# Kernel tuning notes

Hardware: AMD Instinct MI355X
Metric: run time of the kernel (lower is better)

Reference implementation:

```python
import jax, jax.numpy as jnp
import numpy as np

LAMBDA_G, LAMBDA_F, TAU, MIU_NU_OTHER = 1.938, 1.912, 3.5, 0.19
EPS = 1e-8

B, N, C, D = 8, 1000, 4000, 128  # batch, n_points, n_customers, embed_dim


def setup_inputs() -> dict:
    key = jax.random.key(0)
    ks = jax.random.split(key, 12)
    return {
        "embeddings": jax.random.normal(ks[0], (B, N, D), dtype=jnp.float32),
        "chosen_count": jax.random.randint(ks[1], (B, N), 0, 3, dtype=jnp.int32),
        "u_lj_reg": jax.random.uniform(ks[2], (B, N, C), dtype=jnp.float32),
        "u_lj_food": jax.random.uniform(ks[3], (B, N, C), dtype=jnp.float32),
        "u0": jax.random.uniform(ks[4], (B, C), dtype=jnp.float32),
        "pop": jax.random.uniform(ks[5], (B, C, 1), dtype=jnp.float32),
        "delivery_distances_reg_set": jax.random.uniform(ks[6], (B, N, 1), dtype=jnp.float32),
        "delivery_distances_food_set": jax.random.uniform(ks[7], (B, N, 1), dtype=jnp.float32),
        "fixed_cost_point": jax.random.uniform(ks[8], (B, 1, N), dtype=jnp.float32),
        "W": jax.random.normal(ks[9], (D, D), dtype=jnp.float32) * (1.0 / np.sqrt(D)),
        "b": jax.random.normal(ks[10], (D,), dtype=jnp.float32) * 0.01,
    }


def reference(embeddings, chosen_count, u_lj_reg, u_lj_food, u0, pop,
              delivery_distances_reg_set, delivery_distances_food_set,
              fixed_cost_point, W, b):
    batch_size, n_points = chosen_count.shape
    regular = (chosen_count >= 1).astype(jnp.float32)            # [B,N]
    food = (chosen_count >= 2).astype(jnp.float32)
    reg_cand = 1.0 - regular
    food_cand = regular - food

    # bmm(u^T, diag(mask)) == column-scale: u_reg[b,c,j] = u[b,j,c] * mask[b,j]
    u_reg = jnp.swapaxes(u_lj_reg, 1, 2) * reg_cand[:, None, :]   # [B,C,N]
    P_reg = u0[..., None] + u_reg + EPS
    revenue_g = jnp.sum(pop * (u_reg / P_reg) * LAMBDA_G, axis=1)  # [B,N]

    u_food = jnp.swapaxes(u_lj_food, 1, 2) * food_cand[:, None, :]
    P_food = u0[..., None] + u_food + EPS
    revenue_f = jnp.sum(pop * (u_food / P_food) * LAMBDA_F, axis=1)

    fcp = fixed_cost_point.reshape(batch_size, n_points)
    del_reg = TAU * (reg_cand * delivery_distances_reg_set[..., 0]) / 1000.0
    fix_reg = reg_cand * fcp
    del_food = TAU * (food_cand * delivery_distances_food_set[..., 0]) / 1000.0
    fix_food = food_cand * fcp

    revenue = revenue_g + revenue_f
    delivery = del_reg + del_food
    fixed = fix_reg + fix_food
    labor = 0.075 * revenue
    land = 0.005 * revenue
    advantage = revenue * MIU_NU_OTHER - labor - land - delivery - fixed
    reward_improve = jnp.clip(advantage, 0.0) / 100.0

    loc_best_soft = jax.nn.softmax(reward_improve, axis=-1)       # [B,N]
    context = jnp.einsum('bnd,bn->bd', embeddings, loc_best_soft)  # [B,D]
    return context @ W.T + b
```

## Files before the change

kernel.cpp:

```cpp
#include <hip/hip_runtime.h>

#define LAMBDA_G 1.938f
#define LAMBDA_F 1.912f
#define TAU_C    3.5f
#define EPSV     1e-8f

constexpr int B = 8, N = 1000, C = 4000, D = 128;
constexpr int S = 25, RPB = 40, RPT = 5;

__device__ __forceinline__ float waveReduceSum(float v) {
#pragma unroll
    for (int off = 32; off > 0; off >>= 1)
        v += __shfl_down(v, off, 64);
    return v;
}

__device__ __forceinline__ float waveReduceMax(float v) {
#pragma unroll
    for (int off = 32; off > 0; off >>= 1)
        v = fmaxf(v, __shfl_down(v, off, 64));
    return v;
}

__global__ __launch_bounds__(256) void reward_kernel(
    const float* __restrict__ u_reg, const float* __restrict__ u_food,
    const float* __restrict__ u0,    const float* __restrict__ pop,
    const int*   __restrict__ chosen,
    const float* __restrict__ dd_reg, const float* __restrict__ dd_food,
    const float* __restrict__ fcp,   float* __restrict__ reward)
{
    const int bj = blockIdx.x;
    const int b  = bj / N;
    const int t  = threadIdx.x;
    const int cc = chosen[bj];

    if (cc >= 2) {
        if (t == 0) reward[bj] = 0.0f;
        return;
    }

    const float* __restrict__ u    = (cc == 0 ? u_reg : u_food) + (size_t)bj * C;
    const float* __restrict__ u0b  = u0  + (size_t)b * C;
    const float* __restrict__ popb = pop + (size_t)b * C;
    const float  lam = (cc == 0) ? LAMBDA_G : LAMBDA_F;
    const float  dd  = (cc == 0) ? dd_reg[bj] : dd_food[bj];

    float acc = 0.0f;
    const float4* u4  = (const float4*)u;
    const float4* u04 = (const float4*)u0b;
    const float4* p4  = (const float4*)popb;
    for (int c4 = t; c4 < C / 4; c4 += 256) {
        float4 uv = u4[c4];
        float4 ov = u04[c4];
        float4 pv = p4[c4];
        acc += pv.x * uv.x / (ov.x + uv.x + EPSV);
        acc += pv.y * uv.y / (ov.y + uv.y + EPSV);
        acc += pv.z * uv.z / (ov.z + uv.z + EPSV);
        acc += pv.w * uv.w / (ov.w + uv.w + EPSV);
    }

    __shared__ float red[4];
    float ws = waveReduceSum(acc);
    if ((t & 63) == 0) red[t >> 6] = ws;
    __syncthreads();
    if (t == 0) {
        float s       = red[0] + red[1] + red[2] + red[3];
        float revenue = lam * s;
        float delivery = TAU_C * dd * (1.0f / 1000.0f);
        float fixedc   = fcp[bj];
        float adv = revenue * 0.19f - 0.075f * revenue - 0.005f * revenue
                    - delivery - fixedc;
        reward[bj] = fmaxf(adv, 0.0f) * 0.01f;
    }
}

__global__ __launch_bounds__(256) void softmax_kernel(
    const float* __restrict__ reward, float* __restrict__ e_out)
{
    const int b = blockIdx.x;
    const int t = threadIdx.x;

    __shared__ float e[N];
    __shared__ float red[4];

    const float* __restrict__ r = reward + b * N;

    float m = -1e30f;
    for (int j = t; j < N; j += 256) m = fmaxf(m, r[j]);
    m = waveReduceMax(m);
    if ((t & 63) == 0) red[t >> 6] = m;
    __syncthreads();
    const float mx = fmaxf(fmaxf(red[0], red[1]), fmaxf(red[2], red[3]));

    float s = 0.0f;
    for (int j = t; j < N; j += 256) {
        float ev = expf(r[j] - mx);
        e[j] = ev;
        s += ev;
    }
    s = waveReduceSum(s);
    __syncthreads();
    if ((t & 63) == 0) red[t >> 6] = s;
    __syncthreads();
    const float inv = 1.0f / (red[0] + red[1] + red[2] + red[3]);

    for (int j = t; j < N; j += 256)
        e_out[b * N + j] = e[j] * inv;
}

__global__ __launch_bounds__(256) void ctx_partial_kernel(
    const float* __restrict__ e, const float* __restrict__ emb,
    float* __restrict__ partials)
{
    const int blk = blockIdx.x;
    const int b = blk / S, s = blk % S;
    const int t = threadIdx.x;
    const int d4 = t & 31;
    const int rg = t >> 5;

    const float* __restrict__ eb = emb + ((size_t)b * N + s * RPB) * D;
    const float* __restrict__ ev = e + b * N + s * RPB;

    float4 acc = {0.f, 0.f, 0.f, 0.f};
#pragma unroll
    for (int k = 0; k < RPT; ++k) {
        const int j = rg * RPT + k;
        const float w = ev[j];
        const float4 v = ((const float4*)(eb + (size_t)j * D))[d4];
        acc.x += v.x * w; acc.y += v.y * w; acc.z += v.z * w; acc.w += v.w * w;
    }

    __shared__ float lds[8][D];
    *(float4*)&lds[rg][d4 * 4] = acc;
    __syncthreads();
    if (t < D) {
        float sum = 0.f;
#pragma unroll
        for (int g = 0; g < 8; ++g) sum += lds[g][t];
        partials[((size_t)b * S + s) * D + t] = sum;
    }
}

__global__ __launch_bounds__(128) void finalize_kernel(
    const float* __restrict__ partials, const float* __restrict__ Wm,
    const float* __restrict__ bias, float* __restrict__ out)
{
    const int b = blockIdx.x;
    const int t = threadIdx.x;

    __shared__ float ctx[D];
    float sum = 0.f;
#pragma unroll 5
    for (int si = 0; si < S; ++si)
        sum += partials[((size_t)b * S + si) * D + t];
    ctx[t] = sum;
    __syncthreads();

    const float* __restrict__ wr = Wm + t * D;
    float a = bias[t];
#pragma unroll 8
    for (int dd = 0; dd < D; ++dd) a += ctx[dd] * wr[dd];
    out[b * D + t] = a;
}

extern "C" void kernel_launch(void* const* d_in, const int* in_sizes, int n_in,
                              void* d_out, int out_size, void* d_ws, size_t ws_size,
                              hipStream_t stream) {
    const float* emb     = (const float*)d_in[0];
    const int*   chosen  = (const int*)  d_in[1];
    const float* u_reg   = (const float*)d_in[2];
    const float* u_food  = (const float*)d_in[3];
    const float* u0      = (const float*)d_in[4];
    const float* pop     = (const float*)d_in[5];
    const float* dd_reg  = (const float*)d_in[6];
    const float* dd_food = (const float*)d_in[7];
    const float* fcp     = (const float*)d_in[8];
    const float* Wm      = (const float*)d_in[9];
    const float* bias    = (const float*)d_in[10];
    float* out = (float*)d_out;

    float* reward   = (float*)d_ws;
    float* e_probs  = reward + B * N;
    float* partials = e_probs + B * N;

    reward_kernel<<<B * N, 256, 0, stream>>>(u_reg, u_food, u0, pop, chosen,
                                             dd_reg, dd_food, fcp, reward);
    softmax_kernel<<<B, 256, 0, stream>>>(reward, e_probs);
    ctx_partial_kernel<<<B * S, 256, 0, stream>>>(e_probs, emb, partials);
    finalize_kernel<<<B, 128, 0, stream>>>(partials, Wm, bias, out);
}
```

Baseline: 261.8 us.

## Fuse softmax into context reduction without max subtraction; nontemporal u loads

```diff
diff --git a/kernel.cpp b/kernel.cpp
--- a/kernel.cpp
+++ b/kernel.cpp
@@ -8,17 +8,12 @@
 constexpr int B = 8, N = 1000, C = 4000, D = 128;
 constexpr int S = 25, RPB = 40, RPT = 5;
 
+typedef float f4 __attribute__((ext_vector_type(4)));
+
 __device__ __forceinline__ float waveReduceSum(float v) {
 #pragma unroll
     for (int off = 32; off > 0; off >>= 1)
         v += __shfl_down(v, off, 64);
-    return v;
-}
-
-__device__ __forceinline__ float waveReduceMax(float v) {
-#pragma unroll
-    for (int off = 32; off > 0; off >>= 1)
-        v = fmaxf(v, __shfl_down(v, off, 64));
     return v;
 }
 
@@ -46,13 +41,14 @@
     const float  dd  = (cc == 0) ? dd_reg[bj] : dd_food[bj];
 
     float acc = 0.0f;
-    const float4* u4  = (const float4*)u;
-    const float4* u04 = (const float4*)u0b;
-    const float4* p4  = (const float4*)popb;
+    const f4* u4  = (const f4*)u;
+    const f4* u04 = (const f4*)u0b;
+    const f4* p4  = (const f4*)popb;
+#pragma unroll
     for (int c4 = t; c4 < C / 4; c4 += 256) {
-        float4 uv = u4[c4];
-        float4 ov = u04[c4];
-        float4 pv = p4[c4];
+        f4 uv = __builtin_nontemporal_load(u4 + c4);
+        f4 ov = u04[c4];
+        f4 pv = p4[c4];
         acc += pv.x * uv.x / (ov.x + uv.x + EPSV);
         acc += pv.y * uv.y / (ov.y + uv.y + EPSV);
         acc += pv.z * uv.z / (ov.z + uv.z + EPSV);
@@ -74,43 +70,9 @@
     }
 }
 
-__global__ __launch_bounds__(256) void softmax_kernel(
-    const float* __restrict__ reward, float* __restrict__ e_out)
-{
-    const int b = blockIdx.x;
-    const int t = threadIdx.x;
-
-    __shared__ float e[N];
-    __shared__ float red[4];
-
-    const float* __restrict__ r = reward + b * N;
-
-    float m = -1e30f;
-    for (int j = t; j < N; j += 256) m = fmaxf(m, r[j]);
-    m = waveReduceMax(m);
-    if ((t & 63) == 0) red[t >> 6] = m;
-    __syncthreads();
-    const float mx = fmaxf(fmaxf(red[0], red[1]), fmaxf(red[2], red[3]));
-
-    float s = 0.0f;
-    for (int j = t; j < N; j += 256) {
-        float ev = expf(r[j] - mx);
-        e[j] = ev;
-        s += ev;
-    }
-    s = waveReduceSum(s);
-    __syncthreads();
-    if ((t & 63) == 0) red[t >> 6] = s;
-    __syncthreads();
-    const float inv = 1.0f / (red[0] + red[1] + red[2] + red[3]);
-
-    for (int j = t; j < N; j += 256)
-        e_out[b * N + j] = e[j] * inv;
-}
-
 __global__ __launch_bounds__(256) void ctx_partial_kernel(
-    const float* __restrict__ e, const float* __restrict__ emb,
-    float* __restrict__ partials)
+    const float* __restrict__ reward, const float* __restrict__ emb,
+    float* __restrict__ partials, float* __restrict__ psum)
 {
     const int blk = blockIdx.x;
     const int b = blk / S, s = blk % S;
@@ -119,19 +81,22 @@
     const int rg = t >> 5;
 
     const float* __restrict__ eb = emb + ((size_t)b * N + s * RPB) * D;
-    const float* __restrict__ ev = e + b * N + s * RPB;
+    const float* __restrict__ rv = reward + b * N + s * RPB;
 
-    float4 acc = {0.f, 0.f, 0.f, 0.f};
+    __shared__ float esum[RPB];
+
+    f4 acc = {0.f, 0.f, 0.f, 0.f};
 #pragma unroll
     for (int k = 0; k < RPT; ++k) {
         const int j = rg * RPT + k;
-        const float w = ev[j];
-        const float4 v = ((const float4*)(eb + (size_t)j * D))[d4];
-        acc.x += v.x * w; acc.y += v.y * w; acc.z += v.z * w; acc.w += v.w * w;
+        const float w = __expf(rv[j]);
+        if (d4 == 0) esum[j] = w;
+        const f4 v = ((const f4*)(eb + (size_t)j * D))[d4];
+        acc += v * w;
     }
 
     __shared__ float lds[8][D];
-    *(float4*)&lds[rg][d4 * 4] = acc;
+    *(f4*)&lds[rg][d4 * 4] = acc;
     __syncthreads();
     if (t < D) {
         float sum = 0.f;
@@ -139,21 +104,30 @@
         for (int g = 0; g < 8; ++g) sum += lds[g][t];
         partials[((size_t)b * S + s) * D + t] = sum;
     }
+    if (t == 0) {
+        float se = 0.f;
+#pragma unroll
+        for (int j = 0; j < RPB; ++j) se += esum[j];
+        psum[b * S + s] = se;
+    }
 }
 
 __global__ __launch_bounds__(128) void finalize_kernel(
-    const float* __restrict__ partials, const float* __restrict__ Wm,
-    const float* __restrict__ bias, float* __restrict__ out)
+    const float* __restrict__ partials, const float* __restrict__ psum,
+    const float* __restrict__ Wm, const float* __restrict__ bias,
+    float* __restrict__ out)
 {
     const int b = blockIdx.x;
     const int t = threadIdx.x;
 
     __shared__ float ctx[D];
-    float sum = 0.f;
+    float sum = 0.f, se = 0.f;
 #pragma unroll 5
-    for (int si = 0; si < S; ++si)
+    for (int si = 0; si < S; ++si) {
         sum += partials[((size_t)b * S + si) * D + t];
-    ctx[t] = sum;
+        se  += psum[b * S + si];
+    }
+    ctx[t] = sum * (1.0f / se);
     __syncthreads();
 
     const float* __restrict__ wr = Wm + t * D;
@@ -180,12 +154,11 @@
     float* out = (float*)d_out;
 
     float* reward   = (float*)d_ws;
-    float* e_probs  = reward + B * N;
-    float* partials = e_probs + B * N;
+    float* partials = reward + B * N;
+    float* psum     = partials + B * S * D;
 
     reward_kernel<<<B * N, 256, 0, stream>>>(u_reg, u_food, u0, pop, chosen,
                                              dd_reg, dd_food, fcp, reward);
-    softmax_kernel<<<B, 256, 0, stream>>>(reward, e_probs);
-    ctx_partial_kernel<<<B * S, 256, 0, stream>>>(e_probs, emb, partials);
-    finalize_kernel<<<B, 128, 0, stream>>>(partials, Wm, bias, out);
+    ctx_partial_kernel<<<B * S, 256, 0, stream>>>(reward, emb, partials, psum);
+    finalize_kernel<<<B, 128, 0, stream>>>(partials, psum, Wm, bias, out);
 }
```

Result: faster. 253.3 us (-3.2%).
